# Kernel optimization log

Measured on AMD Instinct MI355X. Metric: run time of the kernel, lower is better.

Reference implementation:

```python
import jax, jax.numpy as jnp
import numpy as np

N, E = 50000, 800000
C_IN, C_OUT, HID = 64, 64, 64


def setup_inputs() -> dict:
    key = jax.random.key(0)
    ks = jax.random.split(key, 12)
    def rn(k, shape, scale=0.05):
        return jax.random.normal(k, shape, dtype=jnp.float32) * scale
    return dict(
        x=jax.random.normal(ks[0], (N, C_IN), dtype=jnp.float32),
        pos=jax.random.normal(ks[1], (N, 3), dtype=jnp.float32),
        edge_index=jax.random.randint(ks[2], (2, E), 0, N),
        W_in=rn(ks[3], (C_IN, C_IN)), b_in=jnp.zeros((C_IN,), jnp.float32),
        W_out=rn(ks[4], (C_OUT, C_OUT)), b_out=jnp.zeros((C_OUT,), jnp.float32),
        W_lin=rn(ks[5], (C_OUT, C_IN)),   # PointTransformerConv.lin (value), bias=False
        W_src=rn(ks[6], (C_OUT, C_IN)),   # lin_src, bias=False
        W_dst=rn(ks[7], (C_OUT, C_IN)),   # lin_dst, bias=False
        pos_w1=rn(ks[8], (HID, 3)), pos_b1=jnp.zeros((HID,), jnp.float32),
        pos_w2=rn(ks[9], (C_OUT, HID)), pos_b2=jnp.zeros((C_OUT,), jnp.float32),
        att_w1=rn(ks[10], (HID, C_OUT)), att_b1=jnp.zeros((HID,), jnp.float32),
        att_w2=rn(ks[11], (C_OUT, HID)), att_b2=jnp.zeros((C_OUT,), jnp.float32),
    )


def _mlp2(y, w1, b1, w2, b2):
    # MLP([a, 64, b], batch_norm=False): Linear->ReLU->Linear->ReLU
    y = jax.nn.relu(y @ w1.T + b1)
    return jax.nn.relu(y @ w2.T + b2)


def reference(x, pos, edge_index, W_in, b_in, W_out, b_out, W_lin, W_src, W_dst,
              pos_w1, pos_b1, pos_w2, pos_b2, att_w1, att_b1, att_w2, att_b2):
    n = x.shape[0]
    h = jax.nn.relu(x @ W_in.T + b_in)            # lin_in + relu, (N, C_in)
    v = h @ W_lin.T                                # value projection (N, C_out)
    k_src = h @ W_src.T                            # alpha_j source part
    q_dst = h @ W_dst.T                            # alpha_i dest part
    # PointTransformerConv adds self-loops by default
    loop = jnp.arange(n)
    src = jnp.concatenate([edge_index[0], loop])   # (E+N,)
    dst = jnp.concatenate([edge_index[1], loop])
    # per-edge positional encoding: pos_nn(pos_i - pos_j)
    delta = _mlp2(pos[dst] - pos[src], pos_w1, pos_b1, pos_w2, pos_b2)
    # per-edge attention logits: attn_nn(alpha_i - alpha_j), (E+N, C_out)
    alpha = _mlp2(q_dst[dst] - k_src[src], att_w1, att_b1, att_w2, att_b2)
    # per-destination-node channelwise softmax (self-loops ensure no empty segment)
    amax = jax.ops.segment_max(alpha, dst, num_segments=n)
    ex = jnp.exp(alpha - amax[dst])
    denom = jax.ops.segment_sum(ex, dst, num_segments=n)
    w = ex / (denom[dst] + 1e-16)
    # message = alpha * (x_j + delta); aggregate = sum over neighbors
    out = jax.ops.segment_sum(w * (v[src] + delta), dst, num_segments=n)
    return jax.nn.relu(out @ W_out.T + b_out)
```

## Files before the change

kernel.cpp:

```cpp
#include <hip/hip_runtime.h>
#include <math.h>

#define NN 50000
#define EE 800000
#define ET (EE + NN)
#define C  64
#define NBLK 49

typedef __attribute__((ext_vector_type(8))) _Float16 f16x8;
typedef __attribute__((ext_vector_type(4))) _Float16 f16x4;
typedef __attribute__((ext_vector_type(2))) _Float16 f16x2;
typedef __attribute__((ext_vector_type(4))) float f32x4;

__device__ __forceinline__ f16x2 pk2(float a, float b) {
  return __builtin_bit_cast(f16x2, __builtin_amdgcn_cvt_pkrtz(a, b));
}
__device__ __forceinline__ f16x4 pk4(float a, float b, float c, float d) {
  return __builtin_shufflevector(pk2(a, b), pk2(c, d), 0, 1, 2, 3);
}

__device__ __forceinline__ f16x8 frag_ldh(const _Float16* base, int row,
                                          int kofs) {
  return *(const f16x8*)(base + row * 72 + kofs);
}

__device__ __forceinline__ void load_whf(_Float16* __restrict__ dst,
                                         const float* __restrict__ W, int tid) {
  const int o = tid >> 2;
  const int kc = (tid & 3) * 16;
  const float4* src = (const float4*)(W + o * 64 + kc);
  f16x4* d = (f16x4*)(dst + o * 72 + kc);
#pragma unroll
  for (int u = 0; u < 4; ++u) {
    const float4 w = src[u];
    d[u] = pk4(w.x, w.y, w.z, w.w);
  }
}

__device__ __forceinline__ void gemm64(const float* __restrict__ AT,
                                       const float* __restrict__ WT,
                                       int m0, int o0, float acc[4][4]) {
#pragma unroll 8
  for (int k = 0; k < 64; ++k) {
    const float4 a = *(const float4*)(AT + k * 64 + m0);
    const float4 w = *(const float4*)(WT + k * 64 + o0);
    const float av[4] = {a.x, a.y, a.z, a.w};
    const float wv[4] = {w.x, w.y, w.z, w.w};
#pragma unroll
    for (int i = 0; i < 4; ++i)
#pragma unroll
      for (int j = 0; j < 4; ++j) acc[i][j] = fmaf(av[i], wv[j], acc[i][j]);
  }
}

__device__ __forceinline__ void load_wT(float* __restrict__ dst,
                                        const float* __restrict__ W, int tid) {
  const int o = tid >> 2;
  const int kc = (tid & 3) * 16;
  const float4* src = (const float4*)(W + o * 64 + kc);
#pragma unroll
  for (int u = 0; u < 4; ++u) {
    const float4 wv = src[u];
    const int kb = kc + 4 * u;
    dst[(kb + 0) * 64 + o] = wv.x;
    dst[(kb + 1) * 64 + o] = wv.y;
    dst[(kb + 2) * 64 + o] = wv.z;
    dst[(kb + 3) * 64 + o] = wv.w;
  }
}

__global__ __launch_bounds__(256) void scan_partial(const int* __restrict__ cnt,
                                                    int* __restrict__ bsum) {
  __shared__ int ws[4];
  const int t = threadIdx.x;
  const int base = blockIdx.x * 1024 + t * 4;
  int s = 0;
  if (base + 3 < NN) {
    const int4 v = *(const int4*)(cnt + base);
    s = v.x + v.y + v.z + v.w;
  } else {
#pragma unroll
    for (int i = 0; i < 4; ++i)
      if (base + i < NN) s += cnt[base + i];
  }
#pragma unroll
  for (int off = 32; off; off >>= 1) s += __shfl_down(s, off, 64);
  if ((t & 63) == 0) ws[t >> 6] = s;
  __syncthreads();
  if (t == 0) bsum[blockIdx.x] = ws[0] + ws[1] + ws[2] + ws[3];
}

__global__ __launch_bounds__(256) void scan_final(const int* __restrict__ cnt,
                                                  const int* __restrict__ bsum,
                                                  int* __restrict__ curs) {
  __shared__ int tsum[256];
  __shared__ int sblk[64];
  const int t = threadIdx.x;
  if (t < 64) {
    const int mine = (t < NBLK) ? bsum[t] : 0;
    int v = mine;
#pragma unroll
    for (int off = 1; off < 64; off <<= 1) {
      const int u = __shfl_up(v, off, 64);
      if (t >= off) v += u;
    }
    sblk[t] = v - mine;
  }
  const int base = blockIdx.x * 1024 + t * 4;
  int v[4] = {0, 0, 0, 0};
  if (base + 3 < NN) {
    const int4 x = *(const int4*)(cnt + base);
    v[0] = x.x; v[1] = x.y; v[2] = x.z; v[3] = x.w;
  } else {
#pragma unroll
    for (int i = 0; i < 4; ++i)
      if (base + i < NN) v[i] = cnt[base + i];
  }
  const int s = v[0] + v[1] + v[2] + v[3];
  tsum[t] = s;
  __syncthreads();
  for (int off = 1; off < 256; off <<= 1) {
    const int u = (t >= off) ? tsum[t - off] : 0;
    __syncthreads();
    tsum[t] += u;
    __syncthreads();
  }
  int ex = sblk[blockIdx.x] + tsum[t] - s;
#pragma unroll
  for (int i = 0; i < 4; ++i) {
    if (base + i < NN) curs[base + i] = ex;
    ex += v[i];
  }
}

__global__ void scatter_kernel(const int* __restrict__ ei,
                               int* __restrict__ curs, int2* __restrict__ srt) {
  const int e = blockIdx.x * 256 + threadIdx.x;
  if (e >= ET) return;
  int s, d;
  if (e < EE) {
    s = ei[e];
    d = ei[EE + e];
  } else {
    s = e - EE;
    d = s;
  }
  const int p = atomicAdd(&curs[d], 1);
  srt[p] = make_int2(s, d);
}

__global__ __launch_bounds__(256, 3) void node_proj(
    const float* __restrict__ x, const float* __restrict__ W_in,
    const float* __restrict__ b_in, const float* __restrict__ W_lin,
    const float* __restrict__ W_src, const float* __restrict__ W_dst,
    const int* __restrict__ ei, int* __restrict__ cnt, float* __restrict__ v,
    _Float16* __restrict__ kh, _Float16* __restrict__ qh) {
  __shared__ __align__(16) float bufX[64 * 64];
  __shared__ __align__(16) float bufH[64 * 64];
  __shared__ __align__(16) float wbuf[64 * 64];
  __shared__ __align__(16) float bias[64];

  const int tid = threadIdx.x;
  const int nb = blockIdx.x * 64;
  const int m0 = (tid & 15) * 4;
  const int o0 = (tid >> 4) * 4;

  {
    const int stride = gridDim.x * 256;
    for (int e = blockIdx.x * 256 + tid; e < ET; e += stride) {
      const int d = (e < EE) ? ei[EE + e] : (e - EE);
      atomicAdd(&cnt[d], 1);
    }
  }

  {
    const int n = tid >> 2;
    const int kc = (tid & 3) * 16;
    const int gn = nb + n;
#pragma unroll
    for (int u = 0; u < 4; ++u) {
      float4 xv = make_float4(0.f, 0.f, 0.f, 0.f);
      if (gn < NN) xv = *(const float4*)(x + (size_t)gn * 64 + kc + 4 * u);
      const int kbi = kc + 4 * u;
      bufX[(kbi + 0) * 64 + n] = xv.x;
      bufX[(kbi + 1) * 64 + n] = xv.y;
      bufX[(kbi + 2) * 64 + n] = xv.z;
      bufX[(kbi + 3) * 64 + n] = xv.w;
    }
  }
  load_wT(wbuf, W_in, tid);
  if (tid < 64) bias[tid] = b_in[tid];
  __syncthreads();

  float acc[4][4] = {};
  gemm64(bufX, wbuf, m0, o0, acc);
#pragma unroll
  for (int i = 0; i < 4; ++i)
#pragma unroll
    for (int j = 0; j < 4; ++j) {
      const float h = fmaxf(acc[i][j] + bias[o0 + j], 0.f);
      bufH[(o0 + j) * 64 + (m0 + i)] = h;
    }
  __syncthreads();

  const float* Ws[3] = {W_lin, W_src, W_dst};
#pragma unroll 1
  for (int p = 0; p < 3; ++p) {
    load_wT(wbuf, Ws[p], tid);
    __syncthreads();
    float a2[4][4] = {};
    gemm64(bufH, wbuf, m0, o0, a2);
#pragma unroll
    for (int i = 0; i < 4; ++i) {
      const int gn = nb + m0 + i;
      if (gn < NN) {
        if (p == 0) {
          const float4 r = make_float4(a2[i][0], a2[i][1], a2[i][2], a2[i][3]);
          *(float4*)(v + (size_t)gn * 64 + o0) = r;
        } else {
          _Float16* dst = (p == 1) ? kh : qh;
          *(f16x4*)(dst + (size_t)gn * 64 + o0) =
              pk4(a2[i][0], a2[i][1], a2[i][2], a2[i][3]);
        }
      }
    }
    __syncthreads();
  }
}

__global__ __launch_bounds__(256, 4) void edge_pass(
    const int2* __restrict__ srt, const float* __restrict__ pos,
    const float* __restrict__ vv, const _Float16* __restrict__ kh,
    const _Float16* __restrict__ qh, const float* __restrict__ att_w1,
    const float* __restrict__ att_b1, const float* __restrict__ att_w2,
    const float* __restrict__ att_b2, const float* __restrict__ pos_w1,
    const float* __restrict__ pos_b1, const float* __restrict__ pos_w2,
    const float* __restrict__ pos_b2, float* __restrict__ num,
    float* __restrict__ den) {
  __shared__ __align__(16) _Float16 smem[18432];
  __shared__ __align__(16) float posw1T[3 * 64];
  __shared__ float b1s[64], b2s[64], pb1s[64], pb2s[64];
  __shared__ int dsts[64];

  _Float16* W1  = smem;
  _Float16* W2  = smem + 4608;
  _Float16* PW2 = smem + 9216;
  _Float16* h1  = smem + 13824;
  float2* pairb = (float2*)smem;

  const int tid = threadIdx.x;
  const int eb = blockIdx.x * 64;
  const int l15 = tid & 15;
  const int quad = (tid >> 4) & 3;
  const int wband = tid >> 6;
  const int eloc = wband * 16 + l15;

  int s_mine, d_mine;
  f16x8 bfrag[2];
  float dp0, dp1, dp2;
  {
    const int e = eb + eloc;
    int2 sd = make_int2(0, 0);
    int valid_d = -1;
    if (e < ET) {
      sd = srt[e];
      valid_d = sd.y;
    }
    s_mine = sd.x;
    d_mine = sd.y;
    if (quad == 0) dsts[eloc] = valid_d;
#pragma unroll
    for (int ks = 0; ks < 2; ++ks) {
      const f16x8 qv =
          *(const f16x8*)(qh + (size_t)d_mine * 64 + ks * 32 + quad * 8);
      const f16x8 kv =
          *(const f16x8*)(kh + (size_t)s_mine * 64 + ks * 32 + quad * 8);
      bfrag[ks] = qv - kv;
    }
    dp0 = pos[(size_t)d_mine * 3 + 0] - pos[(size_t)s_mine * 3 + 0];
    dp1 = pos[(size_t)d_mine * 3 + 1] - pos[(size_t)s_mine * 3 + 1];
    dp2 = pos[(size_t)d_mine * 3 + 2] - pos[(size_t)s_mine * 3 + 2];
  }

  load_whf(W1, att_w1, tid);
  load_whf(W2, att_w2, tid);
  load_whf(PW2, pos_w2, tid);
  if (tid < 64) {
    b1s[tid] = att_b1[tid];
    b2s[tid] = att_b2[tid];
    pb1s[tid] = pos_b1[tid];
    pb2s[tid] = pos_b2[tid];
    posw1T[0 * 64 + tid] = pos_w1[tid * 3 + 0];
    posw1T[1 * 64 + tid] = pos_w1[tid * 3 + 1];
    posw1T[2 * 64 + tid] = pos_w1[tid * 3 + 2];
  }
  __syncthreads();

#pragma unroll
  for (int t = 0; t < 4; ++t) {
    f32x4 acc = {0.f, 0.f, 0.f, 0.f};
#pragma unroll
    for (int ks = 0; ks < 2; ++ks) {
      const f16x8 af = frag_ldh(W1, t * 16 + l15, ks * 32 + quad * 8);
      acc = __builtin_amdgcn_mfma_f32_16x16x32_f16(af, bfrag[ks], acc, 0, 0, 0);
    }
    const int hb = t * 16 + quad * 4;
    *(f16x4*)(h1 + eloc * 72 + hb) =
        pk4(fmaxf(acc[0] + b1s[hb + 0], 0.f), fmaxf(acc[1] + b1s[hb + 1], 0.f),
            fmaxf(acc[2] + b1s[hb + 2], 0.f), fmaxf(acc[3] + b1s[hb + 3], 0.f));
  }

  f16x8 hpfrag[2];
#pragma unroll
  for (int ks = 0; ks < 2; ++ks) {
    float hv[8];
#pragma unroll
    for (int j = 0; j < 8; ++j) {
      const int i = ks * 32 + quad * 8 + j;
      float a = pb1s[i];
      a = fmaf(dp0, posw1T[i], a);
      a = fmaf(dp1, posw1T[64 + i], a);
      a = fmaf(dp2, posw1T[128 + i], a);
      hv[j] = fmaxf(a, 0.f);
    }
    const f16x4 lo = pk4(hv[0], hv[1], hv[2], hv[3]);
    const f16x4 hi = pk4(hv[4], hv[5], hv[6], hv[7]);
    hpfrag[ks] = __builtin_shufflevector(lo, hi, 0, 1, 2, 3, 4, 5, 6, 7);
  }
  __syncthreads();

  float ex[16], del[16];
  {
    f16x8 hfrag[2];
#pragma unroll
    for (int ks = 0; ks < 2; ++ks)
      hfrag[ks] = frag_ldh(h1, eloc, ks * 32 + quad * 8);
#pragma unroll
    for (int t = 0; t < 4; ++t) {
      f32x4 acc = {0.f, 0.f, 0.f, 0.f};
#pragma unroll
      for (int ks = 0; ks < 2; ++ks) {
        const f16x8 af = frag_ldh(W2, t * 16 + l15, ks * 32 + quad * 8);
        acc = __builtin_amdgcn_mfma_f32_16x16x32_f16(af, hfrag[ks], acc, 0, 0, 0);
      }
      const int ob = t * 16 + quad * 4;
#pragma unroll
      for (int r = 0; r < 4; ++r)
        ex[t * 4 + r] = __expf(fmaxf(acc[r] + b2s[ob + r], 0.f));
    }
  }
#pragma unroll
  for (int t = 0; t < 4; ++t) {
    f32x4 acc = {0.f, 0.f, 0.f, 0.f};
#pragma unroll
    for (int ks = 0; ks < 2; ++ks) {
      const f16x8 af = frag_ldh(PW2, t * 16 + l15, ks * 32 + quad * 8);
      acc = __builtin_amdgcn_mfma_f32_16x16x32_f16(af, hpfrag[ks], acc, 0, 0, 0);
    }
    const int ob = t * 16 + quad * 4;
#pragma unroll
    for (int r = 0; r < 4; ++r)
      del[t * 4 + r] = fmaxf(acc[r] + pb2s[ob + r], 0.f);
  }
  float vr[16];
#pragma unroll
  for (int t = 0; t < 4; ++t) {
    const float4 v4 =
        *(const float4*)(vv + (size_t)s_mine * 64 + t * 16 + quad * 4);
    vr[t * 4 + 0] = v4.x;
    vr[t * 4 + 1] = v4.y;
    vr[t * 4 + 2] = v4.z;
    vr[t * 4 + 3] = v4.w;
  }
  __syncthreads();

#pragma unroll
  for (int t = 0; t < 4; ++t) {
#pragma unroll
    for (int r = 0; r < 4; ++r) {
      const int o = t * 16 + quad * 4 + r;
      const int sl = (eloc + 2 * o) & 63;
      const float e_ = ex[t * 4 + r];
      pairb[o * 65 + sl] = make_float2(e_ * (vr[t * 4 + r] + del[t * 4 + r]), e_);
    }
  }
  __syncthreads();

  {
    const int c = tid & 63;
    const int r = tid >> 6;
    float am = 0.f, ae = 0.f;
    int cur = -1;
#pragma unroll 1
    for (int t2 = 0; t2 < 16; ++t2) {
      const int el = r * 16 + t2;
      const int d = dsts[el];
      if (d != cur) {
        if (cur >= 0) {
          unsafeAtomicAdd(num + (size_t)cur * 64 + c, am);
          unsafeAtomicAdd(den + (size_t)cur * 64 + c, ae);
        }
        cur = d;
        am = 0.f;
        ae = 0.f;
      }
      if (d >= 0) {
        const float2 pe = pairb[c * 65 + ((el + 2 * c) & 63)];
        am += pe.x;
        ae += pe.y;
      }
    }
    if (cur >= 0) {
      unsafeAtomicAdd(num + (size_t)cur * 64 + c, am);
      unsafeAtomicAdd(den + (size_t)cur * 64 + c, ae);
    }
  }
}

__global__ __launch_bounds__(256, 3) void out_proj(
    const float* __restrict__ num, const float* __restrict__ den,
    const float* __restrict__ W_out, const float* __restrict__ b_out,
    float* __restrict__ out) {
  __shared__ __align__(16) float bufY[64 * 64];
  __shared__ __align__(16) float wbuf[64 * 64];
  __shared__ __align__(16) float bias[64];

  const int tid = threadIdx.x;
  const int nb = blockIdx.x * 64;
  const int m0 = (tid & 15) * 4;
  const int o0 = (tid >> 4) * 4;

  {
    const int n = tid >> 2;
    const int kc = (tid & 3) * 16;
    const int gn = nb + n;
#pragma unroll
    for (int u = 0; u < 4; ++u) {
      float4 nm = make_float4(0.f, 0.f, 0.f, 0.f);
      float4 dn = make_float4(1.f, 1.f, 1.f, 1.f);
      if (gn < NN) {
        nm = *(const float4*)(num + (size_t)gn * 64 + kc + 4 * u);
        dn = *(const float4*)(den + (size_t)gn * 64 + kc + 4 * u);
      }
      const int kbi = kc + 4 * u;
      bufY[(kbi + 0) * 64 + n] = nm.x / (dn.x + 1e-16f);
      bufY[(kbi + 1) * 64 + n] = nm.y / (dn.y + 1e-16f);
      bufY[(kbi + 2) * 64 + n] = nm.z / (dn.z + 1e-16f);
      bufY[(kbi + 3) * 64 + n] = nm.w / (dn.w + 1e-16f);
    }
  }
  load_wT(wbuf, W_out, tid);
  if (tid < 64) bias[tid] = b_out[tid];
  __syncthreads();

  float acc[4][4] = {};
  gemm64(bufY, wbuf, m0, o0, acc);
#pragma unroll
  for (int i = 0; i < 4; ++i) {
    const int gn = nb + m0 + i;
    if (gn < NN) {
      float4 r;
      r.x = fmaxf(acc[i][0] + bias[o0 + 0], 0.f);
      r.y = fmaxf(acc[i][1] + bias[o0 + 1], 0.f);
      r.z = fmaxf(acc[i][2] + bias[o0 + 2], 0.f);
      r.w = fmaxf(acc[i][3] + bias[o0 + 3], 0.f);
      *(float4*)(out + (size_t)gn * 64 + o0) = r;
    }
  }
}

extern "C" void kernel_launch(void* const* d_in, const int* in_sizes, int n_in,
                              void* d_out, int out_size, void* d_ws,
                              size_t ws_size, hipStream_t stream) {
  const float* x      = (const float*)d_in[0];
  const float* pos    = (const float*)d_in[1];
  const int*   ei     = (const int*)d_in[2];
  const float* W_in   = (const float*)d_in[3];
  const float* b_in   = (const float*)d_in[4];
  const float* W_out  = (const float*)d_in[5];
  const float* b_out  = (const float*)d_in[6];
  const float* W_lin  = (const float*)d_in[7];
  const float* W_src  = (const float*)d_in[8];
  const float* W_dst  = (const float*)d_in[9];
  const float* pos_w1 = (const float*)d_in[10];
  const float* pos_b1 = (const float*)d_in[11];
  const float* pos_w2 = (const float*)d_in[12];
  const float* pos_b2 = (const float*)d_in[13];
  const float* att_w1 = (const float*)d_in[14];
  const float* att_b1 = (const float*)d_in[15];
  const float* att_w2 = (const float*)d_in[16];
  const float* att_b2 = (const float*)d_in[17];

  float* ws = (float*)d_ws;
  const size_t NC = (size_t)NN * C;
  float* v   = ws;
  float* num = ws + NC;
  float* den = ws + 2 * NC;
  _Float16* kh = (_Float16*)(ws + 3 * NC);
  _Float16* qh = kh + NC;
  int* ib    = (int*)(qh + NC);
  int* cnt   = ib;
  int* curs  = ib + NN;
  int* bsum  = ib + 2 * NN;
  int2* srt  = (int2*)(((uintptr_t)(bsum + NBLK) + 15) & ~(uintptr_t)15);

  hipMemsetAsync(num, 0, 2 * NC * sizeof(float), stream);
  hipMemsetAsync(cnt, 0, NN * sizeof(int), stream);

  const dim3 blk(256);
  node_proj<<<dim3((NN + 63) / 64), blk, 0, stream>>>(
      x, W_in, b_in, W_lin, W_src, W_dst, ei, cnt, v, kh, qh);
  scan_partial<<<dim3(NBLK), blk, 0, stream>>>(cnt, bsum);
  scan_final<<<dim3(NBLK), blk, 0, stream>>>(cnt, bsum, curs);
  scatter_kernel<<<dim3((ET + 255) / 256), blk, 0, stream>>>(ei, curs, srt);
  edge_pass<<<dim3((ET + 63) / 64), blk, 0, stream>>>(
      srt, pos, v, kh, qh, att_w1, att_b1, att_w2, att_b2, pos_w1, pos_b1,
      pos_w2, pos_b2, num, den);
  out_proj<<<dim3((NN + 63) / 64), blk, 0, stream>>>(num, den, W_out, b_out,
                                                     (float*)d_out);
}
```

Before: 344.5 us.

## Use MFMA for node and output projections, pre-convert weights to fp16

Replaces the scalar fp32 64x64 GEMMs in node_proj and out_proj with f16 MFMA 16x16x32 instructions. A new prep kernel converts all weight matrices to fp16 once per call, and the kernels stage them straight into LDS. The value projection is now stored in fp16, which halves gather traffic in edge_pass. The scatter kernel handles four edges per thread using vector loads. The trade-off is lower precision for h and v and one extra small kernel launch.

```diff
diff --git a/kernel.cpp b/kernel.cpp
--- a/kernel.cpp
+++ b/kernel.cpp
@@ -18,54 +18,39 @@
 __device__ __forceinline__ f16x4 pk4(float a, float b, float c, float d) {
   return __builtin_shufflevector(pk2(a, b), pk2(c, d), 0, 1, 2, 3);
 }
+__device__ __forceinline__ f16x8 pk8(const float* y) {
+  const f16x4 lo = pk4(y[0], y[1], y[2], y[3]);
+  const f16x4 hi = pk4(y[4], y[5], y[6], y[7]);
+  return __builtin_shufflevector(lo, hi, 0, 1, 2, 3, 4, 5, 6, 7);
+}
 
 __device__ __forceinline__ f16x8 frag_ldh(const _Float16* base, int row,
                                           int kofs) {
   return *(const f16x8*)(base + row * 72 + kofs);
 }
 
-__device__ __forceinline__ void load_whf(_Float16* __restrict__ dst,
-                                         const float* __restrict__ W, int tid) {
-  const int o = tid >> 2;
-  const int kc = (tid & 3) * 16;
-  const float4* src = (const float4*)(W + o * 64 + kc);
-  f16x4* d = (f16x4*)(dst + o * 72 + kc);
-#pragma unroll
-  for (int u = 0; u < 4; ++u) {
-    const float4 w = src[u];
-    d[u] = pk4(w.x, w.y, w.z, w.w);
-  }
-}
-
-__device__ __forceinline__ void gemm64(const float* __restrict__ AT,
-                                       const float* __restrict__ WT,
-                                       int m0, int o0, float acc[4][4]) {
-#pragma unroll 8
-  for (int k = 0; k < 64; ++k) {
-    const float4 a = *(const float4*)(AT + k * 64 + m0);
-    const float4 w = *(const float4*)(WT + k * 64 + o0);
-    const float av[4] = {a.x, a.y, a.z, a.w};
-    const float wv[4] = {w.x, w.y, w.z, w.w};
-#pragma unroll
-    for (int i = 0; i < 4; ++i)
-#pragma unroll
-      for (int j = 0; j < 4; ++j) acc[i][j] = fmaf(av[i], wv[j], acc[i][j]);
-  }
-}
-
-__device__ __forceinline__ void load_wT(float* __restrict__ dst,
-                                        const float* __restrict__ W, int tid) {
-  const int o = tid >> 2;
-  const int kc = (tid & 3) * 16;
-  const float4* src = (const float4*)(W + o * 64 + kc);
-#pragma unroll
-  for (int u = 0; u < 4; ++u) {
-    const float4 wv = src[u];
-    const int kb = kc + 4 * u;
-    dst[(kb + 0) * 64 + o] = wv.x;
-    dst[(kb + 1) * 64 + o] = wv.y;
-    dst[(kb + 2) * 64 + o] = wv.z;
-    dst[(kb + 3) * 64 + o] = wv.w;
+__device__ __forceinline__ void stage_w(_Float16* __restrict__ dst,
+                                        const _Float16* __restrict__ src16,
+                                        int tid) {
+  const f16x8* src = (const f16x8*)(src16 + tid * 16);
+  _Float16* d = dst + (tid >> 2) * 72 + (tid & 3) * 16;
+  ((f16x8*)d)[0] = src[0];
+  ((f16x8*)d)[1] = src[1];
+}
+
+__global__ __launch_bounds__(256) void prep_kernel(
+    const float* __restrict__ W_in, const float* __restrict__ W_lin,
+    const float* __restrict__ W_src, const float* __restrict__ W_dst,
+    const float* __restrict__ att_w1, const float* __restrict__ att_w2,
+    const float* __restrict__ pos_w2, const float* __restrict__ W_out,
+    _Float16* __restrict__ w16) {
+  const float* Ws[8] = {W_in, W_lin, W_src, W_dst, att_w1, att_w2, pos_w2, W_out};
+  const float* src = Ws[blockIdx.x];
+  _Float16* dst = w16 + blockIdx.x * 4096;
+#pragma unroll
+  for (int i = threadIdx.x * 4; i < 4096; i += 1024) {
+    const float4 w = *(const float4*)(src + i);
+    *(f16x4*)(dst + i) = pk4(w.x, w.y, w.z, w.w);
   }
 }
 
@@ -135,35 +120,53 @@
 
 __global__ void scatter_kernel(const int* __restrict__ ei,
                                int* __restrict__ curs, int2* __restrict__ srt) {
-  const int e = blockIdx.x * 256 + threadIdx.x;
-  if (e >= ET) return;
-  int s, d;
-  if (e < EE) {
-    s = ei[e];
-    d = ei[EE + e];
+  const int e0 = (blockIdx.x * 256 + threadIdx.x) * 4;
+  if (e0 >= ET) return;
+  int s[4], d[4];
+  if (e0 + 3 < EE) {
+    const int4 sv = *(const int4*)(ei + e0);
+    const int4 dv = *(const int4*)(ei + EE + e0);
+    s[0] = sv.x; s[1] = sv.y; s[2] = sv.z; s[3] = sv.w;
+    d[0] = dv.x; d[1] = dv.y; d[2] = dv.z; d[3] = dv.w;
   } else {
-    s = e - EE;
-    d = s;
-  }
-  const int p = atomicAdd(&curs[d], 1);
-  srt[p] = make_int2(s, d);
+#pragma unroll
+    for (int i = 0; i < 4; ++i) {
+      const int e = e0 + i;
+      if (e < EE) {
+        s[i] = ei[e];
+        d[i] = ei[EE + e];
+      } else if (e < ET) {
+        s[i] = d[i] = e - EE;
+      } else {
+        s[i] = d[i] = -1;
+      }
+    }
+  }
+#pragma unroll
+  for (int i = 0; i < 4; ++i) {
+    if (d[i] >= 0) {
+      const int p = atomicAdd(&curs[d[i]], 1);
+      srt[p] = make_int2(s[i], d[i]);
+    }
+  }
 }
 
 __global__ __launch_bounds__(256, 3) void node_proj(
-    const float* __restrict__ x, const float* __restrict__ W_in,
-    const float* __restrict__ b_in, const float* __restrict__ W_lin,
-    const float* __restrict__ W_src, const float* __restrict__ W_dst,
-    const int* __restrict__ ei, int* __restrict__ cnt, float* __restrict__ v,
+    const float* __restrict__ x, const float* __restrict__ b_in,
+    const _Float16* __restrict__ w16, const int* __restrict__ ei,
+    int* __restrict__ cnt, _Float16* __restrict__ vh,
     _Float16* __restrict__ kh, _Float16* __restrict__ qh) {
-  __shared__ __align__(16) float bufX[64 * 64];
-  __shared__ __align__(16) float bufH[64 * 64];
-  __shared__ __align__(16) float wbuf[64 * 64];
-  __shared__ __align__(16) float bias[64];
+  __shared__ __align__(16) _Float16 wlds[4 * 4608];
+  __shared__ __align__(16) _Float16 hlds[4608];
+  __shared__ float biasv[64];
 
   const int tid = threadIdx.x;
   const int nb = blockIdx.x * 64;
-  const int m0 = (tid & 15) * 4;
-  const int o0 = (tid >> 4) * 4;
+  const int l15 = tid & 15;
+  const int quad = (tid >> 4) & 3;
+  const int wband = tid >> 6;
+  const int nloc = wband * 16 + l15;
+  const int gn = nb + nloc;
 
   {
     const int stride = gridDim.x * 256;
@@ -173,68 +176,70 @@
     }
   }
 
-  {
-    const int n = tid >> 2;
-    const int kc = (tid & 3) * 16;
-    const int gn = nb + n;
-#pragma unroll
-    for (int u = 0; u < 4; ++u) {
-      float4 xv = make_float4(0.f, 0.f, 0.f, 0.f);
-      if (gn < NN) xv = *(const float4*)(x + (size_t)gn * 64 + kc + 4 * u);
-      const int kbi = kc + 4 * u;
-      bufX[(kbi + 0) * 64 + n] = xv.x;
-      bufX[(kbi + 1) * 64 + n] = xv.y;
-      bufX[(kbi + 2) * 64 + n] = xv.z;
-      bufX[(kbi + 3) * 64 + n] = xv.w;
-    }
-  }
-  load_wT(wbuf, W_in, tid);
-  if (tid < 64) bias[tid] = b_in[tid];
-  __syncthreads();
-
-  float acc[4][4] = {};
-  gemm64(bufX, wbuf, m0, o0, acc);
-#pragma unroll
-  for (int i = 0; i < 4; ++i)
-#pragma unroll
-    for (int j = 0; j < 4; ++j) {
-      const float h = fmaxf(acc[i][j] + bias[o0 + j], 0.f);
-      bufH[(o0 + j) * 64 + (m0 + i)] = h;
-    }
-  __syncthreads();
-
-  const float* Ws[3] = {W_lin, W_src, W_dst};
-#pragma unroll 1
+#pragma unroll
+  for (int w = 0; w < 4; ++w) stage_w(wlds + w * 4608, w16 + w * 4096, tid);
+  if (tid < 64) biasv[tid] = b_in[tid];
+
+  f16x8 bfrag[2];
+#pragma unroll
+  for (int ks = 0; ks < 2; ++ks) {
+    float y[8] = {0.f, 0.f, 0.f, 0.f, 0.f, 0.f, 0.f, 0.f};
+    if (gn < NN) {
+      const float4 a = *(const float4*)(x + (size_t)gn * 64 + ks * 32 + quad * 8);
+      const float4 b = *(const float4*)(x + (size_t)gn * 64 + ks * 32 + quad * 8 + 4);
+      y[0] = a.x; y[1] = a.y; y[2] = a.z; y[3] = a.w;
+      y[4] = b.x; y[5] = b.y; y[6] = b.z; y[7] = b.w;
+    }
+    bfrag[ks] = pk8(y);
+  }
+  __syncthreads();
+
+#pragma unroll
+  for (int t = 0; t < 4; ++t) {
+    f32x4 acc = {0.f, 0.f, 0.f, 0.f};
+#pragma unroll
+    for (int ks = 0; ks < 2; ++ks) {
+      const f16x8 af = frag_ldh(wlds, t * 16 + l15, ks * 32 + quad * 8);
+      acc = __builtin_amdgcn_mfma_f32_16x16x32_f16(af, bfrag[ks], acc, 0, 0, 0);
+    }
+    const int hb = t * 16 + quad * 4;
+    *(f16x4*)(hlds + nloc * 72 + hb) =
+        pk4(fmaxf(acc[0] + biasv[hb + 0], 0.f), fmaxf(acc[1] + biasv[hb + 1], 0.f),
+            fmaxf(acc[2] + biasv[hb + 2], 0.f), fmaxf(acc[3] + biasv[hb + 3], 0.f));
+  }
+  __syncthreads();
+
+  f16x8 hfrag[2];
+#pragma unroll
+  for (int ks = 0; ks < 2; ++ks)
+    hfrag[ks] = frag_ldh(hlds, nloc, ks * 32 + quad * 8);
+
+  _Float16* outs[3] = {vh, kh, qh};
+#pragma unroll
   for (int p = 0; p < 3; ++p) {
-    load_wT(wbuf, Ws[p], tid);
-    __syncthreads();
-    float a2[4][4] = {};
-    gemm64(bufH, wbuf, m0, o0, a2);
-#pragma unroll
-    for (int i = 0; i < 4; ++i) {
-      const int gn = nb + m0 + i;
+    const _Float16* W = wlds + (p + 1) * 4608;
+#pragma unroll
+    for (int t = 0; t < 4; ++t) {
+      f32x4 acc = {0.f, 0.f, 0.f, 0.f};
+#pragma unroll
+      for (int ks = 0; ks < 2; ++ks) {
+        const f16x8 af = frag_ldh(W, t * 16 + l15, ks * 32 + quad * 8);
+        acc = __builtin_amdgcn_mfma_f32_16x16x32_f16(af, hfrag[ks], acc, 0, 0, 0);
+      }
       if (gn < NN) {
-        if (p == 0) {
-          const float4 r = make_float4(a2[i][0], a2[i][1], a2[i][2], a2[i][3]);
-          *(float4*)(v + (size_t)gn * 64 + o0) = r;
-        } else {
-          _Float16* dst = (p == 1) ? kh : qh;
-          *(f16x4*)(dst + (size_t)gn * 64 + o0) =
-              pk4(a2[i][0], a2[i][1], a2[i][2], a2[i][3]);
-        }
+        *(f16x4*)(outs[p] + (size_t)gn * 64 + t * 16 + quad * 4) =
+            pk4(acc[0], acc[1], acc[2], acc[3]);
       }
     }
-    __syncthreads();
   }
 }
 
 __global__ __launch_bounds__(256, 4) void edge_pass(
     const int2* __restrict__ srt, const float* __restrict__ pos,
-    const float* __restrict__ vv, const _Float16* __restrict__ kh,
-    const _Float16* __restrict__ qh, const float* __restrict__ att_w1,
-    const float* __restrict__ att_b1, const float* __restrict__ att_w2,
-    const float* __restrict__ att_b2, const float* __restrict__ pos_w1,
-    const float* __restrict__ pos_b1, const float* __restrict__ pos_w2,
+    const _Float16* __restrict__ vh, const _Float16* __restrict__ kh,
+    const _Float16* __restrict__ qh, const _Float16* __restrict__ w16,
+    const float* __restrict__ att_b1, const float* __restrict__ att_b2,
+    const float* __restrict__ pos_w1, const float* __restrict__ pos_b1,
     const float* __restrict__ pos_b2, float* __restrict__ num,
     float* __restrict__ den) {
   __shared__ __align__(16) _Float16 smem[18432];
@@ -282,9 +287,9 @@
     dp2 = pos[(size_t)d_mine * 3 + 2] - pos[(size_t)s_mine * 3 + 2];
   }
 
-  load_whf(W1, att_w1, tid);
-  load_whf(W2, att_w2, tid);
-  load_whf(PW2, pos_w2, tid);
+  stage_w(W1, w16 + 4 * 4096, tid);
+  stage_w(W2, w16 + 5 * 4096, tid);
+  stage_w(PW2, w16 + 6 * 4096, tid);
   if (tid < 64) {
     b1s[tid] = att_b1[tid];
     b2s[tid] = att_b2[tid];
@@ -323,9 +328,7 @@
       a = fmaf(dp2, posw1T[128 + i], a);
       hv[j] = fmaxf(a, 0.f);
     }
-    const f16x4 lo = pk4(hv[0], hv[1], hv[2], hv[3]);
-    const f16x4 hi = pk4(hv[4], hv[5], hv[6], hv[7]);
-    hpfrag[ks] = __builtin_shufflevector(lo, hi, 0, 1, 2, 3, 4, 5, 6, 7);
+    hpfrag[ks] = pk8(hv);
   }
   __syncthreads();
 
@@ -365,12 +368,11 @@
   float vr[16];
 #pragma unroll
   for (int t = 0; t < 4; ++t) {
-    const float4 v4 =
-        *(const float4*)(vv + (size_t)s_mine * 64 + t * 16 + quad * 4);
-    vr[t * 4 + 0] = v4.x;
-    vr[t * 4 + 1] = v4.y;
-    vr[t * 4 + 2] = v4.z;
-    vr[t * 4 + 3] = v4.w;
+    const f16x4 v4 = *(const f16x4*)(vh + (size_t)s_mine * 64 + t * 16 + quad * 4);
+    vr[t * 4 + 0] = (float)v4[0];
+    vr[t * 4 + 1] = (float)v4[1];
+    vr[t * 4 + 2] = (float)v4[2];
+    vr[t * 4 + 3] = (float)v4[3];
   }
   __syncthreads();
 
@@ -417,54 +419,58 @@
   }
 }
 
-__global__ __launch_bounds__(256, 3) void out_proj(
+__global__ __launch_bounds__(256, 4) void out_proj(
     const float* __restrict__ num, const float* __restrict__ den,
-    const float* __restrict__ W_out, const float* __restrict__ b_out,
+    const _Float16* __restrict__ w16, const float* __restrict__ b_out,
     float* __restrict__ out) {
-  __shared__ __align__(16) float bufY[64 * 64];
-  __shared__ __align__(16) float wbuf[64 * 64];
-  __shared__ __align__(16) float bias[64];
+  __shared__ __align__(16) _Float16 wlds[4608];
+  __shared__ float biasv[64];
 
   const int tid = threadIdx.x;
   const int nb = blockIdx.x * 64;
-  const int m0 = (tid & 15) * 4;
-  const int o0 = (tid >> 4) * 4;
-
-  {
-    const int n = tid >> 2;
-    const int kc = (tid & 3) * 16;
-    const int gn = nb + n;
-#pragma unroll
-    for (int u = 0; u < 4; ++u) {
-      float4 nm = make_float4(0.f, 0.f, 0.f, 0.f);
-      float4 dn = make_float4(1.f, 1.f, 1.f, 1.f);
-      if (gn < NN) {
-        nm = *(const float4*)(num + (size_t)gn * 64 + kc + 4 * u);
-        dn = *(const float4*)(den + (size_t)gn * 64 + kc + 4 * u);
-      }
-      const int kbi = kc + 4 * u;
-      bufY[(kbi + 0) * 64 + n] = nm.x / (dn.x + 1e-16f);
-      bufY[(kbi + 1) * 64 + n] = nm.y / (dn.y + 1e-16f);
-      bufY[(kbi + 2) * 64 + n] = nm.z / (dn.z + 1e-16f);
-      bufY[(kbi + 3) * 64 + n] = nm.w / (dn.w + 1e-16f);
-    }
-  }
-  load_wT(wbuf, W_out, tid);
-  if (tid < 64) bias[tid] = b_out[tid];
-  __syncthreads();
-
-  float acc[4][4] = {};
-  gemm64(bufY, wbuf, m0, o0, acc);
-#pragma unroll
-  for (int i = 0; i < 4; ++i) {
-    const int gn = nb + m0 + i;
+  const int l15 = tid & 15;
+  const int quad = (tid >> 4) & 3;
+  const int wband = tid >> 6;
+  const int gn = nb + wband * 16 + l15;
+
+  stage_w(wlds, w16 + 7 * 4096, tid);
+  if (tid < 64) biasv[tid] = b_out[tid];
+
+  f16x8 bfrag[2];
+#pragma unroll
+  for (int ks = 0; ks < 2; ++ks) {
+    float y[8] = {0.f, 0.f, 0.f, 0.f, 0.f, 0.f, 0.f, 0.f};
     if (gn < NN) {
+      const size_t base = (size_t)gn * 64 + ks * 32 + quad * 8;
+      const float4 n0 = *(const float4*)(num + base);
+      const float4 n1 = *(const float4*)(num + base + 4);
+      const float4 d0 = *(const float4*)(den + base);
+      const float4 d1 = *(const float4*)(den + base + 4);
+      y[0] = n0.x / (d0.x + 1e-16f); y[1] = n0.y / (d0.y + 1e-16f);
+      y[2] = n0.z / (d0.z + 1e-16f); y[3] = n0.w / (d0.w + 1e-16f);
+      y[4] = n1.x / (d1.x + 1e-16f); y[5] = n1.y / (d1.y + 1e-16f);
+      y[6] = n1.z / (d1.z + 1e-16f); y[7] = n1.w / (d1.w + 1e-16f);
+    }
+    bfrag[ks] = pk8(y);
+  }
+  __syncthreads();
+
+#pragma unroll
+  for (int t = 0; t < 4; ++t) {
+    f32x4 acc = {0.f, 0.f, 0.f, 0.f};
+#pragma unroll
+    for (int ks = 0; ks < 2; ++ks) {
+      const f16x8 af = frag_ldh(wlds, t * 16 + l15, ks * 32 + quad * 8);
+      acc = __builtin_amdgcn_mfma_f32_16x16x32_f16(af, bfrag[ks], acc, 0, 0, 0);
+    }
+    if (gn < NN) {
+      const int ob = t * 16 + quad * 4;
       float4 r;
-      r.x = fmaxf(acc[i][0] + bias[o0 + 0], 0.f);
-      r.y = fmaxf(acc[i][1] + bias[o0 + 1], 0.f);
-      r.z = fmaxf(acc[i][2] + bias[o0 + 2], 0.f);
-      r.w = fmaxf(acc[i][3] + bias[o0 + 3], 0.f);
-      *(float4*)(out + (size_t)gn * 64 + o0) = r;
+      r.x = fmaxf(acc[0] + biasv[ob + 0], 0.f);
+      r.y = fmaxf(acc[1] + biasv[ob + 1], 0.f);
+      r.z = fmaxf(acc[2] + biasv[ob + 2], 0.f);
+      r.w = fmaxf(acc[3] + biasv[ob + 3], 0.f);
+      *(float4*)(out + (size_t)gn * 64 + ob) = r;
     }
   }
 }
@@ -493,12 +499,13 @@
 
   float* ws = (float*)d_ws;
   const size_t NC = (size_t)NN * C;
-  float* v   = ws;
-  float* num = ws + NC;
-  float* den = ws + 2 * NC;
-  _Float16* kh = (_Float16*)(ws + 3 * NC);
+  float* num = ws;
+  float* den = ws + NC;
+  _Float16* vh = (_Float16*)(ws + 2 * NC);
+  _Float16* kh = vh + NC;
   _Float16* qh = kh + NC;
-  int* ib    = (int*)(qh + NC);
+  _Float16* w16 = qh + NC;
+  int* ib    = (int*)(w16 + 8 * 4096);
   int* cnt   = ib;
   int* curs  = ib + NN;
   int* bsum  = ib + 2 * NN;
@@ -508,14 +515,16 @@
   hipMemsetAsync(cnt, 0, NN * sizeof(int), stream);
 
   const dim3 blk(256);
-  node_proj<<<dim3((NN + 63) / 64), blk, 0, stream>>>(
-      x, W_in, b_in, W_lin, W_src, W_dst, ei, cnt, v, kh, qh);
+  prep_kernel<<<dim3(8), blk, 0, stream>>>(W_in, W_lin, W_src, W_dst, att_w1,
+                                           att_w2, pos_w2, W_out, w16);
+  node_proj<<<dim3((NN + 63) / 64), blk, 0, stream>>>(x, b_in, w16, ei, cnt, vh,
+                                                      kh, qh);
   scan_partial<<<dim3(NBLK), blk, 0, stream>>>(cnt, bsum);
   scan_final<<<dim3(NBLK), blk, 0, stream>>>(cnt, bsum, curs);
-  scatter_kernel<<<dim3((ET + 255) / 256), blk, 0, stream>>>(ei, curs, srt);
+  scatter_kernel<<<dim3((ET + 1023) / 1024), blk, 0, stream>>>(ei, curs, srt);
   edge_pass<<<dim3((ET + 63) / 64), blk, 0, stream>>>(
-      srt, pos, v, kh, qh, att_w1, att_b1, att_w2, att_b2, pos_w1, pos_b1,
-      pos_w2, pos_b2, num, den);
-  out_proj<<<dim3((NN + 63) / 64), blk, 0, stream>>>(num, den, W_out, b_out,
+      srt, pos, vh, kh, qh, w16, att_b1, att_b2, pos_w1, pos_b1, pos_b2, num,
+      den);
+  out_proj<<<dim3((NN + 63) / 64), blk, 0, stream>>>(num, den, w16, b_out,
                                                      (float*)d_out);
 }
```

After: 315.3 us. 1.09x faster.
